# Optimization experiments

Measured on AMD Instinct MI355X. Metric: run time of the kernel, lower is better.

The kernel has to match this reference:

```python
import jax, jax.numpy as jnp
from jax import lax
import numpy as np

K = 3          # kernel_size (must be 3 for shape consistency with the 3x3 sigma conv)
STRIDE = 2
C_IN = 128
EPS = 1e-5     # FrozenBatchNorm2d eps


def setup_inputs() -> dict:
    key = jax.random.key(0)
    k1, k2, k3, k4, k5, k6 = jax.random.split(key, 6)
    x = jax.random.normal(k1, (8, C_IN, 112, 112), dtype=jnp.float32)
    # conv: in_channels -> k*k, 3x3, no bias (kaiming init ~ normal scaled)
    fan_out = K * K * 3 * 3
    conv_w = jax.random.normal(k2, (K * K, C_IN, 3, 3), dtype=jnp.float32) * np.sqrt(2.0 / fan_out)
    bn_w = jax.random.normal(k3, (K * K,), dtype=jnp.float32) * 0.1 + 1.0
    bn_b = jax.random.normal(k4, (K * K,), dtype=jnp.float32) * 0.1
    bn_mean = jax.random.normal(k5, (K * K,), dtype=jnp.float32) * 0.1
    bn_var = jax.random.uniform(k6, (K * K,), dtype=jnp.float32, minval=0.5, maxval=1.5)
    return {"x": x, "conv_w": conv_w, "bn_w": bn_w, "bn_b": bn_b,
            "bn_mean": bn_mean, "bn_var": bn_var}


def _pasa(x, conv_w, bn_w, bn_b, bn_mean, bn_var):
    n, c, h, w = x.shape
    pad = K // 2
    # reflection pad
    xp = jnp.pad(x, ((0, 0), (0, 0), (pad, pad), (pad, pad)), mode="reflect")
    # 3x3 conv, stride 1, VALID on padded input -> same h, w
    sigma = lax.conv_general_dilated(xp, conv_w, (1, 1), "VALID",
                                     dimension_numbers=("NCHW", "OIHW", "NCHW"))
    # frozen BN: affine with fixed running stats
    scale = bn_w / jnp.sqrt(bn_var + EPS)
    shift = bn_b - bn_mean * scale
    sigma = sigma * scale[None, :, None, None] + shift[None, :, None, None]
    sigma = jnp.clip(sigma, 0.0001)                       # clamp min only
    sigma = sigma.reshape(n, 1, K * K, h * w)
    sigma = sigma / jnp.sum(sigma, axis=2, keepdims=True)  # normalize over k*k
    # unfold: k*k shifted views of the padded input (channel-outer, kernel row-major)
    patches = jnp.stack([xp[:, :, i:i + h, j:j + w]
                         for i in range(K) for j in range(K)], axis=2)  # (n,c,9,h,w)
    out = jnp.sum(patches.reshape(n, c, K * K, h * w) * sigma, axis=2).reshape(n, c, h, w)
    return out[:, :, ::STRIDE, ::STRIDE]


def reference(x, conv_w, bn_w, bn_b, bn_mean, bn_var):
    return _pasa(x, conv_w, bn_w, bn_b, bn_mean, bn_var)
```

## Files before the change

kernel.cpp:

```cpp
#include <hip/hip_runtime.h>

#define NB   8
#define C    128
#define H    112
#define W    112
#define HW   (H * W)
#define HO   56
#define WO   56
#define KK   9
#define WAVES 16
#define CPW  8
#define NPAIR (C / 2)
#define PPW  (CPW / 2)
#define WPK_ELEMS (NPAIR * 81)
#define SHIFT_OFF (WPK_ELEMS * 2)

typedef float v2f __attribute__((ext_vector_type(2)));

__global__ void pasa_prep(const float* __restrict__ cw,
                          const float* __restrict__ bw,
                          const float* __restrict__ bb,
                          const float* __restrict__ bm,
                          const float* __restrict__ bv,
                          float* __restrict__ ws) {
    int idx = blockIdx.x * 256 + threadIdx.x;
    if (idx < WPK_ELEMS) {
        int cip = idx / 81;
        int rem = idx % 81;
        int kh = rem / 27;
        int r2 = rem % 27;
        int k  = r2 / 3;
        int kw = r2 % 3;
        float scale = bw[k] / sqrtf(bv[k] + 1e-5f);
        int ca = 2 * cip, cb = 2 * cip + 1;
        ws[2 * idx + 0] = cw[((k * C + ca) * 3 + kh) * 3 + kw] * scale;
        ws[2 * idx + 1] = cw[((k * C + cb) * 3 + kh) * 3 + kw] * scale;
    } else if (idx < WPK_ELEMS + KK) {
        int k = idx - WPK_ELEMS;
        float scale = bw[k] / sqrtf(bv[k] + 1e-5f);
        ws[SHIFT_OFF + k] = bb[k] - bm[k] * scale;
    }
}

__device__ inline v2f pkfma(v2f a, v2f b, v2f c) {
    return __builtin_elementwise_fma(a, b, c);
}

__global__ __launch_bounds__(1024, 4)
void pasa_main(const float* __restrict__ x,
               const v2f* __restrict__ wpk,
               const float* __restrict__ shift,
               float* __restrict__ out) {
    __shared__ float part[WAVES * KK * 64];
    __shared__ float sig[KK * 57];

    const int bid  = blockIdx.x;
    const int n    = bid & 7;
    const int hb   = bid >> 3;
    const int tid  = threadIdx.x;
    const int lane = tid & 63;
    const int wv   = __builtin_amdgcn_readfirstlane(tid >> 6);
    const int wo   = lane < WO ? lane : (WO - 1);

    const int r0 = (hb == 0) ? 1 : (4 * hb - 1);
    const int r1 = 4 * hb;
    const int r2 = 4 * hb + 1;
    const int r3 = 4 * hb + 2;
    const int r4 = 4 * hb + 3;

    const float* xn = x + (size_t)n * C * HW;
    const int p0 = wv * PPW;

    v2f va[PPW][3], vb[PPW][3];
#pragma unroll
    for (int p = 0; p < PPW; ++p) {
        const float* xa = xn + (size_t)(2 * (p0 + p)) * HW + 2 * wo;
        const float* xb = xa + HW;
        va[p][0] = *(const v2f*)(xa + r0 * W);
        va[p][1] = *(const v2f*)(xa + r1 * W);
        va[p][2] = *(const v2f*)(xa + r2 * W);
        vb[p][0] = *(const v2f*)(xb + r0 * W);
        vb[p][1] = *(const v2f*)(xb + r1 * W);
        vb[p][2] = *(const v2f*)(xb + r2 * W);
    }

    v2f ta[PPW][2], tb[PPW][2];
    float* on_base = out + (size_t)n * C * (HO * WO);

#pragma unroll
    for (int half = 0; half < 2; ++half) {
        v2f acc[KK];
#pragma unroll
        for (int k = 0; k < KK; ++k) acc[k] = (v2f){0.0f, 0.0f};

#pragma unroll
        for (int p = 0; p < PPW; ++p) {
            const v2f* wb = wpk + (p0 + p) * 81;
#pragma unroll
            for (int kh = 0; kh < 3; ++kh) {
                v2f t1 = { va[p][kh].x, vb[p][kh].x };
                v2f t2 = { va[p][kh].y, vb[p][kh].y };
                v2f t0;
                t0.x = __shfl_up(t2.x, 1);
                t0.y = __shfl_up(t2.y, 1);
                const v2f* wr = wb + kh * 27;
#pragma unroll
                for (int k = 0; k < KK; ++k)
                    acc[k] = pkfma(t2, wr[3 * k + 2],
                              pkfma(t1, wr[3 * k + 1],
                              pkfma(t0, wr[3 * k + 0], acc[k])));
            }
        }

#pragma unroll
        for (int k = 0; k < KK; ++k)
            part[(wv * KK + k) * 64 + lane] = acc[k].x + acc[k].y;

        if (half == 0) {
#pragma unroll
            for (int p = 0; p < PPW; ++p) {
                const float* xa = xn + (size_t)(2 * (p0 + p)) * HW + 2 * wo;
                const float* xb = xa + HW;
                ta[p][0] = *(const v2f*)(xa + r3 * W);
                ta[p][1] = *(const v2f*)(xa + r4 * W);
                tb[p][0] = *(const v2f*)(xb + r3 * W);
                tb[p][1] = *(const v2f*)(xb + r4 * W);
            }
        }
        __syncthreads();

        if (tid < KK * WO) {
            const int k = tid / WO;
            const int w_ = tid % WO;
            float s = 0.0f;
#pragma unroll
            for (int w2 = 0; w2 < WAVES; ++w2) s += part[(w2 * KK + k) * 64 + w_];
            s += shift[k];
            s = fmaxf(s, 1e-4f);
            sig[k * 57 + w_] = s;
        }
        __syncthreads();

        float sg[KK];
        float tot = 0.0f;
#pragma unroll
        for (int k = 0; k < KK; ++k) { sg[k] = sig[k * 57 + wo]; tot += sg[k]; }
        const float inv = 1.0f / tot;
#pragma unroll
        for (int k = 0; k < KK; ++k) sg[k] *= inv;

        const int ho = 2 * hb + half;
        float* on = on_base + (size_t)ho * WO;
#pragma unroll
        for (int p = 0; p < PPW; ++p) {
            v2f o = (v2f){0.0f, 0.0f};
#pragma unroll
            for (int kh = 0; kh < 3; ++kh) {
                v2f t1 = { va[p][kh].x, vb[p][kh].x };
                v2f t2 = { va[p][kh].y, vb[p][kh].y };
                v2f t0;
                t0.x = __shfl_up(t2.x, 1);
                t0.y = __shfl_up(t2.y, 1);
                v2f s0 = { sg[kh * 3 + 0], sg[kh * 3 + 0] };
                v2f s1 = { sg[kh * 3 + 1], sg[kh * 3 + 1] };
                v2f s2 = { sg[kh * 3 + 2], sg[kh * 3 + 2] };
                o = pkfma(t2, s2, pkfma(t1, s1, pkfma(t0, s0, o)));
            }
            if (lane < WO) {
                const int ci = 2 * (p0 + p);
                __builtin_nontemporal_store(o.x, on + (size_t)ci * (HO * WO) + lane);
                __builtin_nontemporal_store(o.y, on + (size_t)(ci + 1) * (HO * WO) + lane);
            }
        }

        if (half == 0) {
#pragma unroll
            for (int p = 0; p < PPW; ++p) {
                va[p][0] = va[p][2]; va[p][1] = ta[p][0]; va[p][2] = ta[p][1];
                vb[p][0] = vb[p][2]; vb[p][1] = tb[p][0]; vb[p][2] = tb[p][1];
            }
        }
    }
}

extern "C" void kernel_launch(void* const* d_in, const int* in_sizes, int n_in,
                              void* d_out, int out_size, void* d_ws, size_t ws_size,
                              hipStream_t stream) {
    const float* x   = (const float*)d_in[0];
    const float* cw  = (const float*)d_in[1];
    const float* bw  = (const float*)d_in[2];
    const float* bb  = (const float*)d_in[3];
    const float* bm  = (const float*)d_in[4];
    const float* bv  = (const float*)d_in[5];
    float* ws  = (float*)d_ws;
    float* out = (float*)d_out;

    const int prep_elems = WPK_ELEMS + KK;
    pasa_prep<<<(prep_elems + 255) / 256, 256, 0, stream>>>(cw, bw, bb, bm, bv, ws);
    pasa_main<<<NB * (HO / 2), 1024, 0, stream>>>(x, (const v2f*)ws,
                                                  ws + SHIFT_OFF, out);
}
```

Before: 110.3 us.

## Fuse weight prep into main kernel with per-wave LDS weights and early loads

Removes the separate prep kernel: each wave now computes its own BN-scaled packed conv weights from the raw inputs and stores them in LDS, and the BN shift is computed inline during the sigma reduction. Weight reads in the inner loop come from LDS instead of global/scalar memory. The second-half input rows are also loaded up front rather than mid-loop. This saves a kernel launch and its dependency, at the cost of redundant weight prep in every block, about 41 KB of extra LDS per block (which may limit occupancy), and higher register pressure from the early loads.

Result: slower. 124.8 us (+13.1%).

```diff
diff --git a/kernel.cpp b/kernel.cpp
--- a/kernel.cpp
+++ b/kernel.cpp
@@ -12,35 +12,9 @@
 #define CPW  8
 #define NPAIR (C / 2)
 #define PPW  (CPW / 2)
-#define WPK_ELEMS (NPAIR * 81)
-#define SHIFT_OFF (WPK_ELEMS * 2)
+#define WPW  (PPW * 81)
 
 typedef float v2f __attribute__((ext_vector_type(2)));
-
-__global__ void pasa_prep(const float* __restrict__ cw,
-                          const float* __restrict__ bw,
-                          const float* __restrict__ bb,
-                          const float* __restrict__ bm,
-                          const float* __restrict__ bv,
-                          float* __restrict__ ws) {
-    int idx = blockIdx.x * 256 + threadIdx.x;
-    if (idx < WPK_ELEMS) {
-        int cip = idx / 81;
-        int rem = idx % 81;
-        int kh = rem / 27;
-        int r2 = rem % 27;
-        int k  = r2 / 3;
-        int kw = r2 % 3;
-        float scale = bw[k] / sqrtf(bv[k] + 1e-5f);
-        int ca = 2 * cip, cb = 2 * cip + 1;
-        ws[2 * idx + 0] = cw[((k * C + ca) * 3 + kh) * 3 + kw] * scale;
-        ws[2 * idx + 1] = cw[((k * C + cb) * 3 + kh) * 3 + kw] * scale;
-    } else if (idx < WPK_ELEMS + KK) {
-        int k = idx - WPK_ELEMS;
-        float scale = bw[k] / sqrtf(bv[k] + 1e-5f);
-        ws[SHIFT_OFF + k] = bb[k] - bm[k] * scale;
-    }
-}
 
 __device__ inline v2f pkfma(v2f a, v2f b, v2f c) {
     return __builtin_elementwise_fma(a, b, c);
@@ -48,9 +22,13 @@
 
 __global__ __launch_bounds__(1024, 4)
 void pasa_main(const float* __restrict__ x,
-               const v2f* __restrict__ wpk,
-               const float* __restrict__ shift,
+               const float* __restrict__ cw,
+               const float* __restrict__ bw,
+               const float* __restrict__ bb,
+               const float* __restrict__ bm,
+               const float* __restrict__ bv,
                float* __restrict__ out) {
+    __shared__ v2f   wlds[WAVES][WPW];
     __shared__ float part[WAVES * KK * 64];
     __shared__ float sig[KK * 57];
 
@@ -72,6 +50,7 @@
     const int p0 = wv * PPW;
 
     v2f va[PPW][3], vb[PPW][3];
+    v2f ta[PPW][2], tb[PPW][2];
 #pragma unroll
     for (int p = 0; p < PPW; ++p) {
         const float* xa = xn + (size_t)(2 * (p0 + p)) * HW + 2 * wo;
@@ -82,9 +61,27 @@
         vb[p][0] = *(const v2f*)(xb + r0 * W);
         vb[p][1] = *(const v2f*)(xb + r1 * W);
         vb[p][2] = *(const v2f*)(xb + r2 * W);
+        ta[p][0] = *(const v2f*)(xa + r3 * W);
+        ta[p][1] = *(const v2f*)(xa + r4 * W);
+        tb[p][0] = *(const v2f*)(xb + r3 * W);
+        tb[p][1] = *(const v2f*)(xb + r4 * W);
     }
 
-    v2f ta[PPW][2], tb[PPW][2];
+    for (int i = lane; i < WPW; i += 64) {
+        const int p   = i / 81;
+        const int rem = i % 81;
+        const int kh  = rem / 27;
+        const int rr  = rem % 27;
+        const int k   = rr / 3;
+        const int kw  = rr % 3;
+        const float scale = bw[k] * rsqrtf(bv[k] + 1e-5f);
+        const int ca = 2 * (p0 + p);
+        v2f wv2;
+        wv2.x = cw[((k * C + ca)     * 3 + kh) * 3 + kw] * scale;
+        wv2.y = cw[((k * C + ca + 1) * 3 + kh) * 3 + kw] * scale;
+        wlds[wv][i] = wv2;
+    }
+
     float* on_base = out + (size_t)n * C * (HO * WO);
 
 #pragma unroll
@@ -95,7 +92,6 @@
 
 #pragma unroll
         for (int p = 0; p < PPW; ++p) {
-            const v2f* wb = wpk + (p0 + p) * 81;
 #pragma unroll
             for (int kh = 0; kh < 3; ++kh) {
                 v2f t1 = { va[p][kh].x, vb[p][kh].x };
@@ -103,7 +99,7 @@
                 v2f t0;
                 t0.x = __shfl_up(t2.x, 1);
                 t0.y = __shfl_up(t2.y, 1);
-                const v2f* wr = wb + kh * 27;
+                const v2f* wr = &wlds[wv][p * 81 + kh * 27];
 #pragma unroll
                 for (int k = 0; k < KK; ++k)
                     acc[k] = pkfma(t2, wr[3 * k + 2],
@@ -115,27 +111,16 @@
 #pragma unroll
         for (int k = 0; k < KK; ++k)
             part[(wv * KK + k) * 64 + lane] = acc[k].x + acc[k].y;
-
-        if (half == 0) {
-#pragma unroll
-            for (int p = 0; p < PPW; ++p) {
-                const float* xa = xn + (size_t)(2 * (p0 + p)) * HW + 2 * wo;
-                const float* xb = xa + HW;
-                ta[p][0] = *(const v2f*)(xa + r3 * W);
-                ta[p][1] = *(const v2f*)(xa + r4 * W);
-                tb[p][0] = *(const v2f*)(xb + r3 * W);
-                tb[p][1] = *(const v2f*)(xb + r4 * W);
-            }
-        }
         __syncthreads();
 
         if (tid < KK * WO) {
-            const int k = tid / WO;
+            const int k  = tid / WO;
             const int w_ = tid % WO;
             float s = 0.0f;
 #pragma unroll
             for (int w2 = 0; w2 < WAVES; ++w2) s += part[(w2 * KK + k) * 64 + w_];
-            s += shift[k];
+            const float scale = bw[k] * rsqrtf(bv[k] + 1e-5f);
+            s += bb[k] - bm[k] * scale;
             s = fmaxf(s, 1e-4f);
             sig[k * 57 + w_] = s;
         }
@@ -192,11 +177,8 @@
     const float* bb  = (const float*)d_in[3];
     const float* bm  = (const float*)d_in[4];
     const float* bv  = (const float*)d_in[5];
-    float* ws  = (float*)d_ws;
     float* out = (float*)d_out;
+    (void)d_ws; (void)ws_size;
 
-    const int prep_elems = WPK_ELEMS + KK;
-    pasa_prep<<<(prep_elems + 255) / 256, 256, 0, stream>>>(cw, bw, bb, bm, bv, ws);
-    pasa_main<<<NB * (HO / 2), 1024, 0, stream>>>(x, (const v2f*)ws,
-                                                  ws + SHIFT_OFF, out);
+    pasa_main<<<NB * (HO / 2), 1024, 0, stream>>>(x, cw, bw, bb, bm, bv, out);
 }
```

## Process one output row per block to double grid size and raise occupancy

Applied to the files above, without the earlier changes.

Splits each block's work from two output rows to one, doubling the grid and raising the launch-bounds occupancy hint. Input rows are no longer kept in registers across the two phases; the weighting phase reloads them from memory/cache. This aims to fill all compute units and reduce register pressure, at the cost of extra loads of the shared halo row and the reloaded rows. Also swaps a divide-by-sqrt for rsqrt in the prep kernel.

After: 106.7 us. 1.03x faster.

```diff
diff --git a/kernel.cpp b/kernel.cpp
--- a/kernel.cpp
+++ b/kernel.cpp
@@ -9,13 +9,16 @@
 #define WO   56
 #define KK   9
 #define WAVES 16
-#define CPW  8
+#define PPW  4
 #define NPAIR (C / 2)
-#define PPW  (CPW / 2)
 #define WPK_ELEMS (NPAIR * 81)
 #define SHIFT_OFF (WPK_ELEMS * 2)
 
 typedef float v2f __attribute__((ext_vector_type(2)));
+
+__device__ inline v2f pkfma(v2f a, v2f b, v2f c) {
+    return __builtin_elementwise_fma(a, b, c);
+}
 
 __global__ void pasa_prep(const float* __restrict__ cw,
                           const float* __restrict__ bw,
@@ -31,22 +34,18 @@
         int r2 = rem % 27;
         int k  = r2 / 3;
         int kw = r2 % 3;
-        float scale = bw[k] / sqrtf(bv[k] + 1e-5f);
+        float scale = bw[k] * rsqrtf(bv[k] + 1e-5f);
         int ca = 2 * cip, cb = 2 * cip + 1;
         ws[2 * idx + 0] = cw[((k * C + ca) * 3 + kh) * 3 + kw] * scale;
         ws[2 * idx + 1] = cw[((k * C + cb) * 3 + kh) * 3 + kw] * scale;
     } else if (idx < WPK_ELEMS + KK) {
         int k = idx - WPK_ELEMS;
-        float scale = bw[k] / sqrtf(bv[k] + 1e-5f);
+        float scale = bw[k] * rsqrtf(bv[k] + 1e-5f);
         ws[SHIFT_OFF + k] = bb[k] - bm[k] * scale;
     }
 }
 
-__device__ inline v2f pkfma(v2f a, v2f b, v2f c) {
-    return __builtin_elementwise_fma(a, b, c);
-}
-
-__global__ __launch_bounds__(1024, 4)
+__global__ __launch_bounds__(1024, 8)
 void pasa_main(const float* __restrict__ x,
                const v2f* __restrict__ wpk,
                const float* __restrict__ shift,
@@ -56,129 +55,102 @@
 
     const int bid  = blockIdx.x;
     const int n    = bid & 7;
-    const int hb   = bid >> 3;
+    const int ho   = bid >> 3;
     const int tid  = threadIdx.x;
     const int lane = tid & 63;
     const int wv   = __builtin_amdgcn_readfirstlane(tid >> 6);
     const int wo   = lane < WO ? lane : (WO - 1);
 
-    const int r0 = (hb == 0) ? 1 : (4 * hb - 1);
-    const int r1 = 4 * hb;
-    const int r2 = 4 * hb + 1;
-    const int r3 = 4 * hb + 2;
-    const int r4 = 4 * hb + 3;
+    const int r0 = (ho == 0) ? 1 : (2 * ho - 1);
+    const int r1 = 2 * ho;
+    const int r2 = 2 * ho + 1;
 
-    const float* xn = x + (size_t)n * C * HW;
+    const float* xn = x + (size_t)n * C * HW + 2 * wo;
     const int p0 = wv * PPW;
 
-    v2f va[PPW][3], vb[PPW][3];
+    v2f acc[KK];
 #pragma unroll
+    for (int k = 0; k < KK; ++k) acc[k] = (v2f){0.0f, 0.0f};
+
+#pragma unroll 2
     for (int p = 0; p < PPW; ++p) {
-        const float* xa = xn + (size_t)(2 * (p0 + p)) * HW + 2 * wo;
+        const float* xa = xn + (size_t)(2 * (p0 + p)) * HW;
         const float* xb = xa + HW;
-        va[p][0] = *(const v2f*)(xa + r0 * W);
-        va[p][1] = *(const v2f*)(xa + r1 * W);
-        va[p][2] = *(const v2f*)(xa + r2 * W);
-        vb[p][0] = *(const v2f*)(xb + r0 * W);
-        vb[p][1] = *(const v2f*)(xb + r1 * W);
-        vb[p][2] = *(const v2f*)(xb + r2 * W);
+        v2f va0 = *(const v2f*)(xa + r0 * W);
+        v2f va1 = *(const v2f*)(xa + r1 * W);
+        v2f va2 = *(const v2f*)(xa + r2 * W);
+        v2f vb0 = *(const v2f*)(xb + r0 * W);
+        v2f vb1 = *(const v2f*)(xb + r1 * W);
+        v2f vb2 = *(const v2f*)(xb + r2 * W);
+        const v2f* wb = wpk + (p0 + p) * 81;
+        v2f rowa[3] = { va0, va1, va2 };
+        v2f rowb[3] = { vb0, vb1, vb2 };
+#pragma unroll
+        for (int kh = 0; kh < 3; ++kh) {
+            v2f t1 = { rowa[kh].x, rowb[kh].x };
+            v2f t2 = { rowa[kh].y, rowb[kh].y };
+            v2f t0;
+            t0.x = __shfl_up(t2.x, 1);
+            t0.y = __shfl_up(t2.y, 1);
+            const v2f* wr = wb + kh * 27;
+#pragma unroll
+            for (int k = 0; k < KK; ++k)
+                acc[k] = pkfma(t2, wr[3 * k + 2],
+                          pkfma(t1, wr[3 * k + 1],
+                          pkfma(t0, wr[3 * k + 0], acc[k])));
+        }
     }
 
-    v2f ta[PPW][2], tb[PPW][2];
-    float* on_base = out + (size_t)n * C * (HO * WO);
+#pragma unroll
+    for (int k = 0; k < KK; ++k)
+        part[(wv * KK + k) * 64 + lane] = acc[k].x + acc[k].y;
+    __syncthreads();
 
+    if (tid < KK * WO) {
+        const int k  = tid / WO;
+        const int w_ = tid % WO;
+        float s = 0.0f;
 #pragma unroll
-    for (int half = 0; half < 2; ++half) {
-        v2f acc[KK];
+        for (int w2 = 0; w2 < WAVES; ++w2) s += part[(w2 * KK + k) * 64 + w_];
+        s += shift[k];
+        s = fmaxf(s, 1e-4f);
+        sig[k * 57 + w_] = s;
+    }
+    __syncthreads();
+
+    float sg[KK];
+    float tot = 0.0f;
 #pragma unroll
-        for (int k = 0; k < KK; ++k) acc[k] = (v2f){0.0f, 0.0f};
+    for (int k = 0; k < KK; ++k) { sg[k] = sig[k * 57 + wo]; tot += sg[k]; }
+    const float inv = 1.0f / tot;
+#pragma unroll
+    for (int k = 0; k < KK; ++k) sg[k] *= inv;
 
+    float* on = out + ((size_t)n * C) * (HO * WO) + (size_t)ho * WO + lane;
+#pragma unroll 2
+    for (int p = 0; p < PPW; ++p) {
+        const float* xa = xn + (size_t)(2 * (p0 + p)) * HW;
+        const float* xb = xa + HW;
+        v2f o = (v2f){0.0f, 0.0f};
 #pragma unroll
-        for (int p = 0; p < PPW; ++p) {
-            const v2f* wb = wpk + (p0 + p) * 81;
-#pragma unroll
-            for (int kh = 0; kh < 3; ++kh) {
-                v2f t1 = { va[p][kh].x, vb[p][kh].x };
-                v2f t2 = { va[p][kh].y, vb[p][kh].y };
-                v2f t0;
-                t0.x = __shfl_up(t2.x, 1);
-                t0.y = __shfl_up(t2.y, 1);
-                const v2f* wr = wb + kh * 27;
-#pragma unroll
-                for (int k = 0; k < KK; ++k)
-                    acc[k] = pkfma(t2, wr[3 * k + 2],
-                              pkfma(t1, wr[3 * k + 1],
-                              pkfma(t0, wr[3 * k + 0], acc[k])));
-            }
+        for (int kh = 0; kh < 3; ++kh) {
+            const int rr = (kh == 0) ? r0 : (kh == 1) ? r1 : r2;
+            v2f a = *(const v2f*)(xa + rr * W);
+            v2f b = *(const v2f*)(xb + rr * W);
+            v2f t1 = { a.x, b.x };
+            v2f t2 = { a.y, b.y };
+            v2f t0;
+            t0.x = __shfl_up(t2.x, 1);
+            t0.y = __shfl_up(t2.y, 1);
+            v2f s0 = { sg[kh * 3 + 0], sg[kh * 3 + 0] };
+            v2f s1 = { sg[kh * 3 + 1], sg[kh * 3 + 1] };
+            v2f s2 = { sg[kh * 3 + 2], sg[kh * 3 + 2] };
+            o = pkfma(t2, s2, pkfma(t1, s1, pkfma(t0, s0, o)));
         }
-
-#pragma unroll
-        for (int k = 0; k < KK; ++k)
-            part[(wv * KK + k) * 64 + lane] = acc[k].x + acc[k].y;
-
-        if (half == 0) {
-#pragma unroll
-            for (int p = 0; p < PPW; ++p) {
-                const float* xa = xn + (size_t)(2 * (p0 + p)) * HW + 2 * wo;
-                const float* xb = xa + HW;
-                ta[p][0] = *(const v2f*)(xa + r3 * W);
-                ta[p][1] = *(const v2f*)(xa + r4 * W);
-                tb[p][0] = *(const v2f*)(xb + r3 * W);
-                tb[p][1] = *(const v2f*)(xb + r4 * W);
-            }
-        }
-        __syncthreads();
-
-        if (tid < KK * WO) {
-            const int k = tid / WO;
-            const int w_ = tid % WO;
-            float s = 0.0f;
-#pragma unroll
-            for (int w2 = 0; w2 < WAVES; ++w2) s += part[(w2 * KK + k) * 64 + w_];
-            s += shift[k];
-            s = fmaxf(s, 1e-4f);
-            sig[k * 57 + w_] = s;
-        }
-        __syncthreads();
-
-        float sg[KK];
-        float tot = 0.0f;
-#pragma unroll
-        for (int k = 0; k < KK; ++k) { sg[k] = sig[k * 57 + wo]; tot += sg[k]; }
-        const float inv = 1.0f / tot;
-#pragma unroll
-        for (int k = 0; k < KK; ++k) sg[k] *= inv;
-
-        const int ho = 2 * hb + half;
-        float* on = on_base + (size_t)ho * WO;
-#pragma unroll
-        for (int p = 0; p < PPW; ++p) {
-            v2f o = (v2f){0.0f, 0.0f};
-#pragma unroll
-            for (int kh = 0; kh < 3; ++kh) {
-                v2f t1 = { va[p][kh].x, vb[p][kh].x };
-                v2f t2 = { va[p][kh].y, vb[p][kh].y };
-                v2f t0;
-                t0.x = __shfl_up(t2.x, 1);
-                t0.y = __shfl_up(t2.y, 1);
-                v2f s0 = { sg[kh * 3 + 0], sg[kh * 3 + 0] };
-                v2f s1 = { sg[kh * 3 + 1], sg[kh * 3 + 1] };
-                v2f s2 = { sg[kh * 3 + 2], sg[kh * 3 + 2] };
-                o = pkfma(t2, s2, pkfma(t1, s1, pkfma(t0, s0, o)));
-            }
-            if (lane < WO) {
-                const int ci = 2 * (p0 + p);
-                __builtin_nontemporal_store(o.x, on + (size_t)ci * (HO * WO) + lane);
-                __builtin_nontemporal_store(o.y, on + (size_t)(ci + 1) * (HO * WO) + lane);
-            }
-        }
-
-        if (half == 0) {
-#pragma unroll
-            for (int p = 0; p < PPW; ++p) {
-                va[p][0] = va[p][2]; va[p][1] = ta[p][0]; va[p][2] = ta[p][1];
-                vb[p][0] = vb[p][2]; vb[p][1] = tb[p][0]; vb[p][2] = tb[p][1];
-            }
+        if (lane < WO) {
+            const int ci = 2 * (p0 + p);
+            __builtin_nontemporal_store(o.x, on + (size_t)ci * (HO * WO));
+            __builtin_nontemporal_store(o.y, on + (size_t)(ci + 1) * (HO * WO));
         }
     }
 }
@@ -197,6 +169,6 @@
 
     const int prep_elems = WPK_ELEMS + KK;
     pasa_prep<<<(prep_elems + 255) / 256, 256, 0, stream>>>(cw, bw, bb, bm, bv, ws);
-    pasa_main<<<NB * (HO / 2), 1024, 0, stream>>>(x, (const v2f*)ws,
-                                                  ws + SHIFT_OFF, out);
+    pasa_main<<<NB * HO, 1024, 0, stream>>>(x, (const v2f*)ws,
+                                            ws + SHIFT_OFF, out);
 }
```
